# Kernel tuning notes

Hardware: AMD Instinct MI355X
Metric: run time of the kernel (lower is better)

Reference implementation:

```python
import jax, jax.numpy as jnp
import numpy as np

N_NODES = 100000
N_EDGES = 1600000
D = 64
PROP_STEP = 4
RESIDUAL = 1.0


def setup_inputs() -> dict:
    key = jax.random.key(0)
    ks = jax.random.split(key, 6)
    in_feat = jax.random.normal(ks[0], (N_NODES, D), dtype=jnp.float32)
    edge_weight = jax.random.uniform(ks[1], (N_EDGES,), dtype=jnp.float32)
    W1 = jax.random.normal(ks[2], (D, D), dtype=jnp.float32) / np.sqrt(D)
    b1 = jnp.zeros((D,), dtype=jnp.float32)
    W2 = jax.random.normal(ks[3], (D, D), dtype=jnp.float32) / np.sqrt(D)
    b2 = jnp.zeros((D,), dtype=jnp.float32)
    src = jax.random.randint(ks[4], (N_EDGES,), 0, N_NODES, dtype=jnp.int64 if jax.config.jax_enable_x64 else jnp.int32)
    dst = jax.random.randint(ks[5], (N_EDGES,), 0, N_NODES, dtype=jnp.int64 if jax.config.jax_enable_x64 else jnp.int32)
    return {"in_feat": in_feat, "edge_weight": edge_weight, "W1": W1, "b1": b1,
            "W2": W2, "b2": b2, "src": src, "dst": dst}


def _gcn_conv(x, W, b, src, dst, w):
    # GCNConv: out = A_hat @ (x W) + b, A_hat given as weighted edge list
    xw = x @ W                         # [N, D] dense GEMM (small D)
    msg = xw[src] * w[:, None]         # [E, D] gather + scale
    agg = jax.ops.segment_sum(msg, dst, num_segments=N_NODES)  # scatter-add
    return agg + b


def reference(in_feat, edge_weight, W1, b1, W2, b2, src, dst):
    ori = in_feat
    h = _gcn_conv(in_feat, W1, b1, src, dst, edge_weight) + RESIDUAL * ori
    for _ in range(1, PROP_STEP):
        h = _gcn_conv(h, W2, b2, src, dst, edge_weight) + RESIDUAL * ori
    return h
```

## Files before the change

### kernel.cpp

```cpp
#include <hip/hip_runtime.h>
#include <hip/hip_fp16.h>

#define NN 100000
#define NE 1600000
#define D 64
#define NPS 256
#define NS ((NN + NPS - 1) / NPS)
#define CAPS 4608
#define P1_BLOCKS 256
#define P1_T 1024
#define P1_CH (NE / P1_BLOCKS)

typedef __attribute__((ext_vector_type(8))) _Float16 half8;
typedef __attribute__((ext_vector_type(4))) _Float16 half4_t;
typedef __attribute__((ext_vector_type(4))) float f32x4;

__global__ void __launch_bounds__(256) gemm64_f32(const float* __restrict__ x,
                                                  const float* __restrict__ W,
                                                  __half* __restrict__ out,
                                                  __half* __restrict__ xh, int n) {
    __shared__ _Float16 sWT[64][72];
    int tid = threadIdx.x;
    for (int i = tid; i < 64 * 64; i += 256) {
        int k = i >> 6, c = i & 63;
        sWT[c][k] = (_Float16)W[i];
    }
    __syncthreads();
    int lane = tid & 63;
    int wid  = tid >> 6;
    int lrow = lane & 15;
    int kslc = lane >> 4;

    half8 bfrag[4][2];
#pragma unroll
    for (int t = 0; t < 4; ++t)
#pragma unroll
        for (int kb = 0; kb < 2; ++kb)
            bfrag[t][kb] = *(const half8*)&sWT[t * 16 + lrow][kb * 32 + kslc * 8];

    int nstrips = (n + 15) >> 4;
    for (int s = blockIdx.x * 4 + wid; s < nstrips; s += gridDim.x * 4) {
        int row = s * 16 + lrow;
        half8 a0 = {}, a1 = {};
        if (row < n) {
            const float* p = x + (size_t)row * 64 + kslc * 8;
            float4 u0 = *(const float4*)p;
            float4 u1 = *(const float4*)(p + 4);
            float4 u2 = *(const float4*)(p + 32);
            float4 u3 = *(const float4*)(p + 36);
            a0 = (half8){(_Float16)u0.x, (_Float16)u0.y, (_Float16)u0.z, (_Float16)u0.w,
                         (_Float16)u1.x, (_Float16)u1.y, (_Float16)u1.z, (_Float16)u1.w};
            a1 = (half8){(_Float16)u2.x, (_Float16)u2.y, (_Float16)u2.z, (_Float16)u2.w,
                         (_Float16)u3.x, (_Float16)u3.y, (_Float16)u3.z, (_Float16)u3.w};
            *(half8*)(xh + (size_t)row * 64 + kslc * 8) = a0;
            *(half8*)(xh + (size_t)row * 64 + 32 + kslc * 8) = a1;
        }
        f32x4 acc0 = {0.f, 0.f, 0.f, 0.f}, acc1 = acc0, acc2 = acc0, acc3 = acc0;
        acc0 = __builtin_amdgcn_mfma_f32_16x16x32_f16(a0, bfrag[0][0], acc0, 0, 0, 0);
        acc0 = __builtin_amdgcn_mfma_f32_16x16x32_f16(a1, bfrag[0][1], acc0, 0, 0, 0);
        acc1 = __builtin_amdgcn_mfma_f32_16x16x32_f16(a0, bfrag[1][0], acc1, 0, 0, 0);
        acc1 = __builtin_amdgcn_mfma_f32_16x16x32_f16(a1, bfrag[1][1], acc1, 0, 0, 0);
        acc2 = __builtin_amdgcn_mfma_f32_16x16x32_f16(a0, bfrag[2][0], acc2, 0, 0, 0);
        acc2 = __builtin_amdgcn_mfma_f32_16x16x32_f16(a1, bfrag[2][1], acc2, 0, 0, 0);
        acc3 = __builtin_amdgcn_mfma_f32_16x16x32_f16(a0, bfrag[3][0], acc3, 0, 0, 0);
        acc3 = __builtin_amdgcn_mfma_f32_16x16x32_f16(a1, bfrag[3][1], acc3, 0, 0, 0);

        int grow0 = s * 16 + kslc * 4;
#pragma unroll
        for (int j = 0; j < 4; ++j) {
            int grow = grow0 + j;
            if (grow < n) {
                __half* o = out + (size_t)grow * 64 + lrow;
                o[0]  = __float2half(acc0[j]);
                o[16] = __float2half(acc1[j]);
                o[32] = __float2half(acc2[j]);
                o[48] = __float2half(acc3[j]);
            }
        }
    }
}

__global__ void __launch_bounds__(256) gemm64_h(const __half* __restrict__ x,
                                                const float* __restrict__ W,
                                                __half* __restrict__ out, int n) {
    __shared__ _Float16 sWT[64][72];
    int tid = threadIdx.x;
    for (int i = tid; i < 64 * 64; i += 256) {
        int k = i >> 6, c = i & 63;
        sWT[c][k] = (_Float16)W[i];
    }
    __syncthreads();
    int lane = tid & 63;
    int wid  = tid >> 6;
    int lrow = lane & 15;
    int kslc = lane >> 4;

    half8 bfrag[4][2];
#pragma unroll
    for (int t = 0; t < 4; ++t)
#pragma unroll
        for (int kb = 0; kb < 2; ++kb)
            bfrag[t][kb] = *(const half8*)&sWT[t * 16 + lrow][kb * 32 + kslc * 8];

    int nstrips = (n + 15) >> 4;
    for (int s = blockIdx.x * 4 + wid; s < nstrips; s += gridDim.x * 4) {
        int row = s * 16 + lrow;
        half8 a0 = {}, a1 = {};
        if (row < n) {
            const __half* p = x + (size_t)row * 64 + kslc * 8;
            a0 = *(const half8*)p;
            a1 = *(const half8*)(p + 32);
        }
        f32x4 acc0 = {0.f, 0.f, 0.f, 0.f}, acc1 = acc0, acc2 = acc0, acc3 = acc0;
        acc0 = __builtin_amdgcn_mfma_f32_16x16x32_f16(a0, bfrag[0][0], acc0, 0, 0, 0);
        acc0 = __builtin_amdgcn_mfma_f32_16x16x32_f16(a1, bfrag[0][1], acc0, 0, 0, 0);
        acc1 = __builtin_amdgcn_mfma_f32_16x16x32_f16(a0, bfrag[1][0], acc1, 0, 0, 0);
        acc1 = __builtin_amdgcn_mfma_f32_16x16x32_f16(a1, bfrag[1][1], acc1, 0, 0, 0);
        acc2 = __builtin_amdgcn_mfma_f32_16x16x32_f16(a0, bfrag[2][0], acc2, 0, 0, 0);
        acc2 = __builtin_amdgcn_mfma_f32_16x16x32_f16(a1, bfrag[2][1], acc2, 0, 0, 0);
        acc3 = __builtin_amdgcn_mfma_f32_16x16x32_f16(a0, bfrag[3][0], acc3, 0, 0, 0);
        acc3 = __builtin_amdgcn_mfma_f32_16x16x32_f16(a1, bfrag[3][1], acc3, 0, 0, 0);

        int grow0 = s * 16 + kslc * 4;
#pragma unroll
        for (int j = 0; j < 4; ++j) {
            int grow = grow0 + j;
            if (grow < n) {
                __half* o = out + (size_t)grow * 64 + lrow;
                o[0]  = __float2half(acc0[j]);
                o[16] = __float2half(acc1[j]);
                o[32] = __float2half(acc2[j]);
                o[48] = __float2half(acc3[j]);
            }
        }
    }
}

__global__ void zero_scnt(int* __restrict__ scnt) {
    int t = threadIdx.x;
    if (t < NS) scnt[t] = 0;
}

__global__ void __launch_bounds__(P1_T) super_append(
        const int* __restrict__ src, const int* __restrict__ dst,
        const float* __restrict__ w, int* __restrict__ scnt,
        int2* __restrict__ tmp) {
    __shared__ int hist[NS];
    __shared__ int loff[512];
    __shared__ int gres[NS];
    __shared__ int slotL[P1_CH];
    __shared__ int2 payL[P1_CH];
    int tid = threadIdx.x;
    int e0 = blockIdx.x * P1_CH;
    int e1 = e0 + P1_CH;

    for (int t = tid; t < NS; t += P1_T) hist[t] = 0;
    __syncthreads();
    for (int e = e0 + tid; e < e1; e += P1_T)
        atomicAdd(&hist[dst[e] >> 8], 1);
    __syncthreads();
    if (tid < 512) loff[tid] = (tid < NS) ? hist[tid] : 0;
    __syncthreads();
    for (int off = 1; off < 512; off <<= 1) {
        int x = (tid < 512 && tid >= off) ? loff[tid - off] : 0;
        __syncthreads();
        if (tid < 512) loff[tid] += x;
        __syncthreads();
    }
    if (tid < NS) {
        int h = hist[tid];
        gres[tid] = h ? atomicAdd(&scnt[tid], h) : 0;
        loff[tid] -= h;
        hist[tid] = 0;
    }
    __syncthreads();
    for (int e = e0 + tid; e < e1; e += P1_T) {
        int d = dst[e];
        int s = d >> 8;
        int r = atomicAdd(&hist[s], 1);
        int p = loff[s] + r;
        int g = gres[s] + r;
        int w0 = src[e] | ((d & (NPS - 1)) << 17);
        payL[p] = make_int2(w0, __float_as_int(w[e]));
        slotL[p] = (g < CAPS) ? (s * CAPS + g) : -1;
    }
    __syncthreads();
    for (int p = tid; p < P1_CH; p += P1_T) {
        int g = slotL[p];
        if (g >= 0) tmp[g] = payL[p];
    }
}

__global__ void scan_supers(const int* __restrict__ scnt, int* __restrict__ sbase,
                            int* __restrict__ offsets) {
    __shared__ int s[512];
    int t = threadIdx.x;
    int v = (t < NS) ? min(scnt[t], CAPS) : 0;
    s[t] = v;
    __syncthreads();
    for (int off = 1; off < 512; off <<= 1) {
        int x = (t >= off) ? s[t - off] : 0;
        __syncthreads();
        s[t] += x;
        __syncthreads();
    }
    if (t < NS) sbase[t] = s[t] - v;
    if (t == 511) offsets[NN] = s[511];
}

__global__ void __launch_bounds__(512) super_sort(
        const int2* __restrict__ tmp, const int* __restrict__ scnt,
        const int* __restrict__ sbase, int* __restrict__ offsets,
        unsigned* __restrict__ sew) {
    __shared__ int hcnt[NPS];
    __shared__ int hoff[NPS];
    __shared__ unsigned pay[CAPS];
    int b = blockIdx.x;
    int tid = threadIdx.x;
    int c = min(scnt[b], CAPS);
    const int2* in = tmp + (size_t)b * CAPS;

    if (tid < NPS) hcnt[tid] = 0;
    __syncthreads();
    for (int i = tid; i < c; i += 512)
        atomicAdd(&hcnt[(in[i].x >> 17) & (NPS - 1)], 1);
    __syncthreads();
    if (tid < NPS) hoff[tid] = hcnt[tid];
    __syncthreads();
    for (int off = 1; off < NPS; off <<= 1) {
        int x = (tid < NPS && tid >= off) ? hoff[tid - off] : 0;
        __syncthreads();
        if (tid < NPS) hoff[tid] += x;
        __syncthreads();
    }
    int base = sbase[b];
    if (tid < NPS) {
        int ex = hoff[tid] - hcnt[tid];
        int gnode = b * NPS + tid;
        if (gnode < NN) offsets[gnode] = base + ex;
        hoff[tid] = ex;
        hcnt[tid] = 0;
    }
    __syncthreads();
    for (int i = tid; i < c; i += 512) {
        int2 e = in[i];
        int dl = (e.x >> 17) & (NPS - 1);
        int s = e.x & 0x1FFFF;
        float wv = __int_as_float(e.y);
        int wq = __float2int_rn(wv * 32768.f);
        if (wq > 32767) wq = 32767;
        int r = atomicAdd(&hcnt[dl], 1);
        pay[hoff[dl] + r] = (unsigned)s | ((unsigned)wq << 17);
    }
    __syncthreads();
    for (int i = tid; i < c; i += 512) sew[base + i] = pay[i];
}

__global__ void pull_agg(const __half* __restrict__ xw, const unsigned* __restrict__ sew,
                         const int* __restrict__ offsets,
                         const __half* __restrict__ orih, const float* __restrict__ b,
                         __half* __restrict__ hout, float* __restrict__ fout, int n) {
    const float WS = 1.f / 32768.f;
    int tid = threadIdx.x;
    int lane = tid & 63;
    int g  = lane >> 4;
    int fl = lane & 15;
    int gwave = (int)((blockIdx.x * blockDim.x + tid) >> 6);
    int nw = (int)((gridDim.x * blockDim.x) >> 6);
    float4 bias = *(const float4*)&b[fl * 4];

    for (int v = gwave; v < n; v += nw) {
        int e0 = offsets[v];
        int e1 = offsets[v + 1];
        float ax = 0.f, ay = 0.f, az = 0.f, aw = 0.f;
        for (int base = e0; base < e1; base += 64) {
            int m = e1 - base;
            if (m > 64) m = 64;
            unsigned my = (lane < m) ? sew[base + lane] : 0u;
            int nit = (m + 3) >> 2;
            int j = 0;
            for (; j + 4 <= nit; j += 4) {
                unsigned p0 = __shfl(my, (j + 0) * 4 + g, 64);
                unsigned p1 = __shfl(my, (j + 1) * 4 + g, 64);
                unsigned p2 = __shfl(my, (j + 2) * 4 + g, 64);
                unsigned p3 = __shfl(my, (j + 3) * 4 + g, 64);
                half4_t h0 = *(const half4_t*)(xw + (size_t)(p0 & 0x1FFFF) * D + fl * 4);
                half4_t h1 = *(const half4_t*)(xw + (size_t)(p1 & 0x1FFFF) * D + fl * 4);
                half4_t h2 = *(const half4_t*)(xw + (size_t)(p2 & 0x1FFFF) * D + fl * 4);
                half4_t h3 = *(const half4_t*)(xw + (size_t)(p3 & 0x1FFFF) * D + fl * 4);
                float w0 = (float)(p0 >> 17) * WS;
                float w1 = (float)(p1 >> 17) * WS;
                float w2 = (float)(p2 >> 17) * WS;
                float w3 = (float)(p3 >> 17) * WS;
                ax = fmaf((float)h0.x, w0, ax); ay = fmaf((float)h0.y, w0, ay);
                az = fmaf((float)h0.z, w0, az); aw = fmaf((float)h0.w, w0, aw);
                ax = fmaf((float)h1.x, w1, ax); ay = fmaf((float)h1.y, w1, ay);
                az = fmaf((float)h1.z, w1, az); aw = fmaf((float)h1.w, w1, aw);
                ax = fmaf((float)h2.x, w2, ax); ay = fmaf((float)h2.y, w2, ay);
                az = fmaf((float)h2.z, w2, az); aw = fmaf((float)h2.w, w2, aw);
                ax = fmaf((float)h3.x, w3, ax); ay = fmaf((float)h3.y, w3, ay);
                az = fmaf((float)h3.z, w3, az); aw = fmaf((float)h3.w, w3, aw);
            }
            for (; j < nit; ++j) {
                unsigned p = __shfl(my, j * 4 + g, 64);
                half4_t h = *(const half4_t*)(xw + (size_t)(p & 0x1FFFF) * D + fl * 4);
                float wj = (float)(p >> 17) * WS;
                ax = fmaf((float)h.x, wj, ax); ay = fmaf((float)h.y, wj, ay);
                az = fmaf((float)h.z, wj, az); aw = fmaf((float)h.w, wj, aw);
            }
        }
        ax += __shfl_xor(ax, 16, 64); ax += __shfl_xor(ax, 32, 64);
        ay += __shfl_xor(ay, 16, 64); ay += __shfl_xor(ay, 32, 64);
        az += __shfl_xor(az, 16, 64); az += __shfl_xor(az, 32, 64);
        aw += __shfl_xor(aw, 16, 64); aw += __shfl_xor(aw, 32, 64);
        if (g == 0) {
            half4_t o4 = *(const half4_t*)(orih + (size_t)v * D + fl * 4);
            float rx = ax + bias.x + (float)o4.x;
            float ry = ay + bias.y + (float)o4.y;
            float rz = az + bias.z + (float)o4.z;
            float rw = aw + bias.w + (float)o4.w;
            if (fout) {
                float4 r = {rx, ry, rz, rw};
                *(float4*)&fout[(size_t)v * D + fl * 4] = r;
            } else {
                half4_t r = {(_Float16)rx, (_Float16)ry, (_Float16)rz, (_Float16)rw};
                *(half4_t*)&hout[(size_t)v * D + fl * 4] = r;
            }
        }
    }
}

extern "C" void kernel_launch(void* const* d_in, const int* in_sizes, int n_in,
                              void* d_out, int out_size, void* d_ws, size_t ws_size,
                              hipStream_t stream) {
    const float* in_feat = (const float*)d_in[0];
    const float* ew      = (const float*)d_in[1];
    const float* W1      = (const float*)d_in[2];
    const float* b1      = (const float*)d_in[3];
    const float* W2      = (const float*)d_in[4];
    const float* b2      = (const float*)d_in[5];
    const int*   src     = (const int*)d_in[6];
    const int*   dst     = (const int*)d_in[7];
    float* out = (float*)d_out;

    char* base = (char*)d_ws;
    int2*     tmp     = (int2*)base;
    __half*   hh      = (__half*)(base + (size_t)NS * CAPS * 8);
    __half*   xw      = hh + (size_t)NN * D;
    __half*   orih    = xw + (size_t)NN * D;
    unsigned* sew     = (unsigned*)(orih + (size_t)NN * D);
    int*      scnt    = (int*)(sew + NE);
    int*      sbase   = scnt + NS;
    int*      offsets = sbase + NS;

    zero_scnt<<<1, 512, 0, stream>>>(scnt);
    super_append<<<P1_BLOCKS, P1_T, 0, stream>>>(src, dst, ew, scnt, tmp);
    scan_supers<<<1, 512, 0, stream>>>(scnt, sbase, offsets);
    super_sort<<<NS, 512, 0, stream>>>(tmp, scnt, sbase, offsets, sew);

    gemm64_f32<<<512, 256, 0, stream>>>(in_feat, W1, xw, orih, NN);
    pull_agg<<<4096, 256, 0, stream>>>(xw, sew, offsets, orih, b1, hh, nullptr, NN);

    for (int s = 0; s < 2; ++s) {
        gemm64_h<<<512, 256, 0, stream>>>(hh, W2, xw, NN);
        pull_agg<<<4096, 256, 0, stream>>>(xw, sew, offsets, orih, b2, hh, nullptr, NN);
    }

    gemm64_h<<<512, 256, 0, stream>>>(hh, W2, xw, NN);
    pull_agg<<<4096, 256, 0, stream>>>(xw, sew, offsets, orih, b2, nullptr, out, NN);
}
```

Baseline: 219.5 us.

## Partition edges by source tile and process tiles in lockstep for cache locality

The sort now keys edges by (source tile of 25000 nodes, destination node), giving per-node offsets for each of 4 source tiles. The aggregation kernel gives each 16-lane group four destination nodes and walks source tiles in order across two chunks per block, so that concurrently running blocks gather from the same source tile and the gathered xw rows stay cache-resident. Lanes now read their own edge words directly rather than taking them by shuffle. The costs are a 4x larger offset table, serial per-node loops with load imbalance, and a grid of only 1024 blocks.

Result: slower. 445.5 us (+103.0%).

```diff
diff --git a/kernel.cpp b/kernel.cpp
--- a/kernel.cpp
+++ b/kernel.cpp
@@ -10,6 +10,10 @@
 #define P1_BLOCKS 256
 #define P1_T 1024
 #define P1_CH (NE / P1_BLOCKS)
+#define NT 4
+#define NKEY (NT * NPS)
+#define CHUNKS (NS * 4)
+#define PG 1024
 
 typedef __attribute__((ext_vector_type(8))) _Float16 half8;
 typedef __attribute__((ext_vector_type(4))) _Float16 half4_t;
@@ -192,7 +196,7 @@
 }
 
 __global__ void scan_supers(const int* __restrict__ scnt, int* __restrict__ sbase,
-                            int* __restrict__ offsets) {
+                            int* __restrict__ off2) {
     __shared__ int s[512];
     int t = threadIdx.x;
     int v = (t < NS) ? min(scnt[t], CAPS) : 0;
@@ -205,129 +209,146 @@
         __syncthreads();
     }
     if (t < NS) sbase[t] = s[t] - v;
-    if (t == 511) offsets[NN] = s[511];
+    if (t == 511) off2[NS * NKEY] = s[511];
 }
 
 __global__ void __launch_bounds__(512) super_sort(
         const int2* __restrict__ tmp, const int* __restrict__ scnt,
-        const int* __restrict__ sbase, int* __restrict__ offsets,
+        const int* __restrict__ sbase, int* __restrict__ off2,
         unsigned* __restrict__ sew) {
-    __shared__ int hcnt[NPS];
-    __shared__ int hoff[NPS];
+    __shared__ int hcnt[NKEY];
+    __shared__ int hoff[NKEY];
     __shared__ unsigned pay[CAPS];
     int b = blockIdx.x;
     int tid = threadIdx.x;
     int c = min(scnt[b], CAPS);
     const int2* in = tmp + (size_t)b * CAPS;
-
-    if (tid < NPS) hcnt[tid] = 0;
-    __syncthreads();
-    for (int i = tid; i < c; i += 512)
-        atomicAdd(&hcnt[(in[i].x >> 17) & (NPS - 1)], 1);
-    __syncthreads();
-    if (tid < NPS) hoff[tid] = hcnt[tid];
-    __syncthreads();
-    for (int off = 1; off < NPS; off <<= 1) {
-        int x = (tid < NPS && tid >= off) ? hoff[tid - off] : 0;
-        __syncthreads();
-        if (tid < NPS) hoff[tid] += x;
+    int i0 = tid, i1 = tid + 512;
+
+    hcnt[i0] = 0; hcnt[i1] = 0;
+    __syncthreads();
+    for (int i = tid; i < c; i += 512) {
+        int w0 = in[i].x;
+        int s = w0 & 0x1FFFF;
+        int dl = (w0 >> 17) & (NPS - 1);
+        int t = (int)((unsigned)s / 25000u);
+        atomicAdd(&hcnt[t * NPS + dl], 1);
+    }
+    __syncthreads();
+    hoff[i0] = hcnt[i0]; hoff[i1] = hcnt[i1];
+    __syncthreads();
+    for (int off = 1; off < NKEY; off <<= 1) {
+        int x0 = (i0 >= off) ? hoff[i0 - off] : 0;
+        int x1 = (i1 >= off) ? hoff[i1 - off] : 0;
+        __syncthreads();
+        hoff[i0] += x0; hoff[i1] += x1;
         __syncthreads();
     }
     int base = sbase[b];
-    if (tid < NPS) {
-        int ex = hoff[tid] - hcnt[tid];
-        int gnode = b * NPS + tid;
-        if (gnode < NN) offsets[gnode] = base + ex;
-        hoff[tid] = ex;
-        hcnt[tid] = 0;
-    }
+    int e0a = hoff[i0] - hcnt[i0];
+    int e1a = hoff[i1] - hcnt[i1];
+    off2[b * NKEY + i0] = base + e0a;
+    off2[b * NKEY + i1] = base + e1a;
+    hcnt[i0] = e0a; hcnt[i1] = e1a;
     __syncthreads();
     for (int i = tid; i < c; i += 512) {
         int2 e = in[i];
+        int s = e.x & 0x1FFFF;
         int dl = (e.x >> 17) & (NPS - 1);
-        int s = e.x & 0x1FFFF;
+        int t = (int)((unsigned)s / 25000u);
         float wv = __int_as_float(e.y);
         int wq = __float2int_rn(wv * 32768.f);
         if (wq > 32767) wq = 32767;
-        int r = atomicAdd(&hcnt[dl], 1);
-        pay[hoff[dl] + r] = (unsigned)s | ((unsigned)wq << 17);
+        int r = atomicAdd(&hcnt[t * NPS + dl], 1);
+        pay[r] = (unsigned)s | ((unsigned)wq << 17);
     }
     __syncthreads();
     for (int i = tid; i < c; i += 512) sew[base + i] = pay[i];
 }
 
-__global__ void pull_agg(const __half* __restrict__ xw, const unsigned* __restrict__ sew,
-                         const int* __restrict__ offsets,
-                         const __half* __restrict__ orih, const float* __restrict__ b,
-                         __half* __restrict__ hout, float* __restrict__ fout, int n) {
+#define EDGE_FMA(u)                                                            \
+    {                                                                          \
+        half4_t hv = *(const half4_t*)(xw + (size_t)((u) & 0x1FFFF) * D + fl * 4); \
+        float wv = (float)((u) >> 17) * WS;                                    \
+        ac.x = fmaf((float)hv.x, wv, ac.x);                                    \
+        ac.y = fmaf((float)hv.y, wv, ac.y);                                    \
+        ac.z = fmaf((float)hv.z, wv, ac.z);                                    \
+        ac.w = fmaf((float)hv.w, wv, ac.w);                                    \
+    }
+
+__device__ __forceinline__ void proc_chunk_phase(
+        const __half* __restrict__ xw, const unsigned* __restrict__ sew,
+        const int* __restrict__ off2, int c, int t, int gid, int fl,
+        float4 (&acc)[4]) {
     const float WS = 1.f / 32768.f;
-    int tid = threadIdx.x;
-    int lane = tid & 63;
-    int g  = lane >> 4;
-    int fl = lane & 15;
-    int gwave = (int)((blockIdx.x * blockDim.x + tid) >> 6);
-    int nw = (int)((gridDim.x * blockDim.x) >> 6);
+    int S = c >> 2, q = c & 3;
+    int idxb = S * NKEY + t * NPS + q * 64 + gid * 4;
+#pragma unroll
+    for (int i = 0; i < 4; ++i) {
+        int e0 = off2[idxb + i];
+        int e1 = off2[idxb + i + 1];
+        float4 ac = acc[i];
+        int e = e0;
+        for (; e + 4 <= e1; e += 4) {
+            unsigned u0 = sew[e], u1 = sew[e + 1], u2 = sew[e + 2], u3 = sew[e + 3];
+            EDGE_FMA(u0); EDGE_FMA(u1); EDGE_FMA(u2); EDGE_FMA(u3);
+        }
+        for (; e < e1; ++e) {
+            unsigned u = sew[e];
+            EDGE_FMA(u);
+        }
+        acc[i] = ac;
+    }
+}
+
+__device__ __forceinline__ void write_chunk(
+        const __half* __restrict__ orih, const float4 bias,
+        __half* __restrict__ hout, float* __restrict__ fout,
+        int c, int gid, int fl, float4 (&acc)[4]) {
+    int S = c >> 2, q = c & 3;
+    int v0 = S * NPS + q * 64 + gid * 4;
+#pragma unroll
+    for (int i = 0; i < 4; ++i) {
+        int v = v0 + i;
+        if (v >= NN) continue;
+        half4_t o4 = *(const half4_t*)(orih + (size_t)v * D + fl * 4);
+        float rx = acc[i].x + bias.x + (float)o4.x;
+        float ry = acc[i].y + bias.y + (float)o4.y;
+        float rz = acc[i].z + bias.z + (float)o4.z;
+        float rw = acc[i].w + bias.w + (float)o4.w;
+        if (fout) {
+            float4 r = {rx, ry, rz, rw};
+            *(float4*)&fout[(size_t)v * D + fl * 4] = r;
+        } else {
+            half4_t r = {(_Float16)rx, (_Float16)ry, (_Float16)rz, (_Float16)rw};
+            *(half4_t*)&hout[(size_t)v * D + fl * 4] = r;
+        }
+    }
+}
+
+__global__ void __launch_bounds__(256) pull_agg(
+        const __half* __restrict__ xw, const unsigned* __restrict__ sew,
+        const int* __restrict__ off2, const __half* __restrict__ orih,
+        const float* __restrict__ b, __half* __restrict__ hout,
+        float* __restrict__ fout) {
+    int tid = threadIdx.x;
+    int gid = tid >> 4;
+    int fl  = tid & 15;
+    int c0 = blockIdx.x;
+    int c1 = c0 + PG;
+    bool has1 = (c1 < CHUNKS);
     float4 bias = *(const float4*)&b[fl * 4];
 
-    for (int v = gwave; v < n; v += nw) {
-        int e0 = offsets[v];
-        int e1 = offsets[v + 1];
-        float ax = 0.f, ay = 0.f, az = 0.f, aw = 0.f;
-        for (int base = e0; base < e1; base += 64) {
-            int m = e1 - base;
-            if (m > 64) m = 64;
-            unsigned my = (lane < m) ? sew[base + lane] : 0u;
-            int nit = (m + 3) >> 2;
-            int j = 0;
-            for (; j + 4 <= nit; j += 4) {
-                unsigned p0 = __shfl(my, (j + 0) * 4 + g, 64);
-                unsigned p1 = __shfl(my, (j + 1) * 4 + g, 64);
-                unsigned p2 = __shfl(my, (j + 2) * 4 + g, 64);
-                unsigned p3 = __shfl(my, (j + 3) * 4 + g, 64);
-                half4_t h0 = *(const half4_t*)(xw + (size_t)(p0 & 0x1FFFF) * D + fl * 4);
-                half4_t h1 = *(const half4_t*)(xw + (size_t)(p1 & 0x1FFFF) * D + fl * 4);
-                half4_t h2 = *(const half4_t*)(xw + (size_t)(p2 & 0x1FFFF) * D + fl * 4);
-                half4_t h3 = *(const half4_t*)(xw + (size_t)(p3 & 0x1FFFF) * D + fl * 4);
-                float w0 = (float)(p0 >> 17) * WS;
-                float w1 = (float)(p1 >> 17) * WS;
-                float w2 = (float)(p2 >> 17) * WS;
-                float w3 = (float)(p3 >> 17) * WS;
-                ax = fmaf((float)h0.x, w0, ax); ay = fmaf((float)h0.y, w0, ay);
-                az = fmaf((float)h0.z, w0, az); aw = fmaf((float)h0.w, w0, aw);
-                ax = fmaf((float)h1.x, w1, ax); ay = fmaf((float)h1.y, w1, ay);
-                az = fmaf((float)h1.z, w1, az); aw = fmaf((float)h1.w, w1, aw);
-                ax = fmaf((float)h2.x, w2, ax); ay = fmaf((float)h2.y, w2, ay);
-                az = fmaf((float)h2.z, w2, az); aw = fmaf((float)h2.w, w2, aw);
-                ax = fmaf((float)h3.x, w3, ax); ay = fmaf((float)h3.y, w3, ay);
-                az = fmaf((float)h3.z, w3, az); aw = fmaf((float)h3.w, w3, aw);
-            }
-            for (; j < nit; ++j) {
-                unsigned p = __shfl(my, j * 4 + g, 64);
-                half4_t h = *(const half4_t*)(xw + (size_t)(p & 0x1FFFF) * D + fl * 4);
-                float wj = (float)(p >> 17) * WS;
-                ax = fmaf((float)h.x, wj, ax); ay = fmaf((float)h.y, wj, ay);
-                az = fmaf((float)h.z, wj, az); aw = fmaf((float)h.w, wj, aw);
-            }
-        }
-        ax += __shfl_xor(ax, 16, 64); ax += __shfl_xor(ax, 32, 64);
-        ay += __shfl_xor(ay, 16, 64); ay += __shfl_xor(ay, 32, 64);
-        az += __shfl_xor(az, 16, 64); az += __shfl_xor(az, 32, 64);
-        aw += __shfl_xor(aw, 16, 64); aw += __shfl_xor(aw, 32, 64);
-        if (g == 0) {
-            half4_t o4 = *(const half4_t*)(orih + (size_t)v * D + fl * 4);
-            float rx = ax + bias.x + (float)o4.x;
-            float ry = ay + bias.y + (float)o4.y;
-            float rz = az + bias.z + (float)o4.z;
-            float rw = aw + bias.w + (float)o4.w;
-            if (fout) {
-                float4 r = {rx, ry, rz, rw};
-                *(float4*)&fout[(size_t)v * D + fl * 4] = r;
-            } else {
-                half4_t r = {(_Float16)rx, (_Float16)ry, (_Float16)rz, (_Float16)rw};
-                *(half4_t*)&hout[(size_t)v * D + fl * 4] = r;
-            }
-        }
-    }
+    float4 accA[4] = {{0,0,0,0},{0,0,0,0},{0,0,0,0},{0,0,0,0}};
+    float4 accB[4] = {{0,0,0,0},{0,0,0,0},{0,0,0,0},{0,0,0,0}};
+
+#pragma unroll
+    for (int t = 0; t < NT; ++t) {
+        proc_chunk_phase(xw, sew, off2, c0, t, gid, fl, accA);
+        if (has1) proc_chunk_phase(xw, sew, off2, c1, t, gid, fl, accB);
+    }
+    write_chunk(orih, bias, hout, fout, c0, gid, fl, accA);
+    if (has1) write_chunk(orih, bias, hout, fout, c1, gid, fl, accB);
 }
 
 extern "C" void kernel_launch(void* const* d_in, const int* in_sizes, int n_in,
@@ -351,21 +372,21 @@
     unsigned* sew     = (unsigned*)(orih + (size_t)NN * D);
     int*      scnt    = (int*)(sew + NE);
     int*      sbase   = scnt + NS;
-    int*      offsets = sbase + NS;
+    int*      off2    = sbase + NS;
 
     zero_scnt<<<1, 512, 0, stream>>>(scnt);
     super_append<<<P1_BLOCKS, P1_T, 0, stream>>>(src, dst, ew, scnt, tmp);
-    scan_supers<<<1, 512, 0, stream>>>(scnt, sbase, offsets);
-    super_sort<<<NS, 512, 0, stream>>>(tmp, scnt, sbase, offsets, sew);
+    scan_supers<<<1, 512, 0, stream>>>(scnt, sbase, off2);
+    super_sort<<<NS, 512, 0, stream>>>(tmp, scnt, sbase, off2, sew);
 
     gemm64_f32<<<512, 256, 0, stream>>>(in_feat, W1, xw, orih, NN);
-    pull_agg<<<4096, 256, 0, stream>>>(xw, sew, offsets, orih, b1, hh, nullptr, NN);
+    pull_agg<<<PG, 256, 0, stream>>>(xw, sew, off2, orih, b1, hh, nullptr);
 
     for (int s = 0; s < 2; ++s) {
         gemm64_h<<<512, 256, 0, stream>>>(hh, W2, xw, NN);
-        pull_agg<<<4096, 256, 0, stream>>>(xw, sew, offsets, orih, b2, hh, nullptr, NN);
+        pull_agg<<<PG, 256, 0, stream>>>(xw, sew, off2, orih, b2, hh, nullptr);
     }
 
     gemm64_h<<<512, 256, 0, stream>>>(hh, W2, xw, NN);
-    pull_agg<<<4096, 256, 0, stream>>>(xw, sew, offsets, orih, b2, nullptr, out, NN);
-}
+    pull_agg<<<PG, 256, 0, stream>>>(xw, sew, off2, orih, b2, nullptr, out);
+}
```
